# Performance work log

Hardware: AMD Instinct MI355X
Metric: run time of the kernel (lower is better)

The kernel has to match this reference:

```python
import jax, jax.numpy as jnp
import numpy as np

N_STREAM = 5
N_ITER = 5
P_DIMS = [240, 240, 240, 240, 240]
P = sum(P_DIMS)          # 1200
B = 128
KAPPA = 0.8
LEAKY_SLOPE = 0.01       # torch nn.LeakyReLU default


def _build_masks():
    # retrive_it_mask=True: mask[i] = ones over first sum(P_DIMS[:n_stream-i]) dims, zeros after
    rows = []
    for i in range(N_ITER):
        n_on = int(sum(P_DIMS[:N_STREAM - i]))
        rows.append(np.concatenate([np.ones(n_on, np.float32), np.zeros(P - n_on, np.float32)]))
    return jnp.asarray(np.stack(rows))  # [n_iter, P]


def f_p(x):
    # LeakyReLU(clamp(x, -1, 1))
    return jax.nn.leaky_relu(jnp.clip(x, -1.0, 1.0), negative_slope=LEAKY_SLOPE)


def setup_inputs() -> dict:
    key = jax.random.key(0)
    k1, k2 = jax.random.split(key)
    query = jax.random.normal(k1, (B, P), dtype=jnp.float32)
    # scale M so the batched GEMV doesn't saturate the clamp everywhere
    M = jax.random.normal(k2, (B, P, P), dtype=jnp.float32) * (1.0 / np.sqrt(P))
    masks = _build_masks()
    return {"query": query, "M": M, "masks": masks}


def reference(query, M, masks):
    # query: [B, P] (torch.cat of the per-stream list), M: [B, P, P], masks: [n_iter, P]
    h = f_p(query)

    def step(h, mask):
        mv = jnp.einsum('bp,bpq->bq', h, M)            # batched vector-matrix product
        h_new = (1.0 - mask) * h + mask * f_p(KAPPA * h + h * mv)
        return h_new, None

    h, _ = jax.lax.scan(step, h, masks)
    # original returns the per-stream split [h[:, n_p[f]:n_p[f+1]]]; that is a zero-cost
    # view of the concatenated h, so we return the full [B, P] tensor.
    return h
```

## Files before the change

### kernel.cpp

```cpp
#include <hip/hip_runtime.h>

namespace {

constexpr int kB = 128;
constexpr int kP = 1200;
constexpr int kP4 = kP / 4;
constexpr float kKappa = 0.8f;
constexpr float kSlope = 0.01f;

constexpr int kZMax = 16;
constexpr int kBatch = 5;

__device__ __forceinline__ float f_p(float x) {
    x = fminf(1.0f, fmaxf(-1.0f, x));
    return x >= 0.0f ? x : kSlope * x;
}

__global__ __launch_bounds__(256) void init_h(const float* __restrict__ q,
                                              float* __restrict__ h) {
    int i = blockIdx.x * 256 + threadIdx.x;
    if (i < kB * kP) h[i] = f_p(q[i]);
}

__global__ __launch_bounds__(256) void mv_partial(const float* __restrict__ h_in,
                                                  const float* __restrict__ M,
                                                  float* __restrict__ part,
                                                  int n_on, int chunk) {
    const int b = blockIdx.y;
    const int z = blockIdx.z;
    const int tile = blockIdx.x;
    const int tid = threadIdx.x;
    const int wave = tid >> 6;
    const int lane = tid & 63;

    __shared__ float hs[kP / 4 + 4];
    __shared__ float4 red[4][64];

    if ((chunk & 3) == 0) {
        const float4* h4 = (const float4*)(h_in + (size_t)b * kP + z * chunk);
        float4* hs4 = (float4*)hs;
        for (int i = tid; i < chunk / 4; i += 256) hs4[i] = h4[i];
    } else {
        const float* hp = h_in + (size_t)b * kP + z * chunk;
        for (int i = tid; i < chunk; i += 256) hs[i] = hp[i];
    }
    __syncthreads();

    const int cf_max = n_on / 4 - 1;
    const int cf = min(tile * 64 + lane, cf_max);

    const int r0 = (chunk * wave) / 4;
    const int r1 = (chunk * (wave + 1)) / 4;

    const float4* Mp = (const float4*)(M + (size_t)b * kP * kP) +
                       (size_t)(z * chunk + r0) * kP4 + cf;

    float4 acc = make_float4(0.f, 0.f, 0.f, 0.f);
    int r = r0;
    for (; r + kBatch <= r1; r += kBatch) {
        float4 m[kBatch];
        #pragma unroll
        for (int j = 0; j < kBatch; ++j) m[j] = Mp[(size_t)j * kP4];
        float hv[kBatch];
        #pragma unroll
        for (int j = 0; j < kBatch; ++j) hv[j] = hs[r + j];
        #pragma unroll
        for (int j = 0; j < kBatch; ++j) {
            acc.x = fmaf(hv[j], m[j].x, acc.x);
            acc.y = fmaf(hv[j], m[j].y, acc.y);
            acc.z = fmaf(hv[j], m[j].z, acc.z);
            acc.w = fmaf(hv[j], m[j].w, acc.w);
        }
        Mp += (size_t)kBatch * kP4;
    }
    for (; r < r1; ++r) {
        float4 m = *Mp;
        float hv = hs[r];
        acc.x = fmaf(hv, m.x, acc.x);
        acc.y = fmaf(hv, m.y, acc.y);
        acc.z = fmaf(hv, m.z, acc.z);
        acc.w = fmaf(hv, m.w, acc.w);
        Mp += kP4;
    }
    red[wave][lane] = acc;
    __syncthreads();

    const int q = tile * 256 + tid;
    if (q < n_on) {
        const float* pf = (const float*)red;
        float mv = pf[0 * 256 + tid] + pf[1 * 256 + tid] +
                   pf[2 * 256 + tid] + pf[3 * 256 + tid];
        part[((size_t)z * kB + b) * kP + q] = mv;
    }
}

__global__ __launch_bounds__(256) void apply_update(const float* __restrict__ h_in,
                                                    const float* __restrict__ part,
                                                    float* __restrict__ h_out,
                                                    int n_on, int nZ) {
    int i = blockIdx.x * 256 + threadIdx.x;
    if (i >= kB * kP) return;
    const int b = i / kP;
    const int q = i - b * kP;
    float h = h_in[i];
    if (q < n_on) {
        float mv = 0.0f;
        for (int z = 0; z < nZ; ++z)
            mv += part[((size_t)z * kB + b) * kP + q];
        h = f_p(kKappa * h + h * mv);
    }
    h_out[i] = h;
}

__global__ __launch_bounds__(256) void iter_step(const float* __restrict__ h_in,
                                                 const float* __restrict__ M,
                                                 float* __restrict__ h_out,
                                                 int n_on) {
    const int b = blockIdx.y;
    const int tile = blockIdx.x;
    const int tid = threadIdx.x;
    const int wave = tid >> 6;
    const int lane = tid & 63;

    __shared__ float hs[kP];
    __shared__ float4 part[4][64];

    {
        const float4* h4 = (const float4*)(h_in + (size_t)b * kP);
        float4* hs4 = (float4*)hs;
        for (int i = tid; i < kP / 4; i += 256) hs4[i] = h4[i];
    }
    __syncthreads();

    if (tile == 0) {
        for (int i = n_on + tid; i < kP; i += 256)
            h_out[(size_t)b * kP + i] = hs[i];
    }

    const int cf_raw = tile * 64 + lane;
    const int cf = min(cf_raw, kP / 4 - 1);
    const int p0 = wave * 300;

    const float4* Mp = (const float4*)(M + (size_t)b * kP * kP) +
                       (size_t)p0 * (kP / 4) + cf;

    float4 acc = make_float4(0.f, 0.f, 0.f, 0.f);
    for (int pb = 0; pb < 300; pb += 12) {
        float4 m[12];
        #pragma unroll
        for (int j = 0; j < 12; ++j) m[j] = Mp[(size_t)j * (kP / 4)];
        float hv[12];
        #pragma unroll
        for (int j = 0; j < 3; ++j) {
            float4 h4v = *(const float4*)&hs[p0 + pb + j * 4];
            hv[j * 4 + 0] = h4v.x; hv[j * 4 + 1] = h4v.y;
            hv[j * 4 + 2] = h4v.z; hv[j * 4 + 3] = h4v.w;
        }
        #pragma unroll
        for (int j = 0; j < 12; ++j) {
            acc.x = fmaf(hv[j], m[j].x, acc.x);
            acc.y = fmaf(hv[j], m[j].y, acc.y);
            acc.z = fmaf(hv[j], m[j].z, acc.z);
            acc.w = fmaf(hv[j], m[j].w, acc.w);
        }
        Mp += 12 * (kP / 4);
    }
    part[wave][lane] = acc;
    __syncthreads();

    const int q = tile * 256 + tid;
    if (q < n_on) {
        const float* pf = (const float*)part;
        float mv = pf[0 * 256 + tid] + pf[1 * 256 + tid] +
                   pf[2 * 256 + tid] + pf[3 * 256 + tid];
        const float hq = hs[q];
        h_out[(size_t)b * kP + q] = f_p(kKappa * hq + hq * mv);
    }
}

}

extern "C" void kernel_launch(void* const* d_in, const int* in_sizes, int n_in,
                              void* d_out, int out_size, void* d_ws, size_t ws_size,
                              hipStream_t stream) {
    const float* query = (const float*)d_in[0];
    const float* M     = (const float*)d_in[1];
    float* out = (float*)d_out;
    float* w   = (float*)d_ws;

    const int n_on[5] = {1200, 960, 720, 480, 240};
    const size_t kHElems = (size_t)kB * kP;
    const size_t kNeed16 = (size_t)(1 + kZMax) * kHElems * sizeof(float);
    const size_t kNeed4  = (size_t)(1 + 4)     * kHElems * sizeof(float);

    init_h<<<dim3((kB * kP + 255) / 256), dim3(256), 0, stream>>>(query, w);

    if (ws_size >= kNeed4) {
        int zs[5] = {4, 4, 6, 8, 16};
        if (ws_size < kNeed16) { zs[2] = 4; zs[3] = 4; zs[4] = 4; }

        float* hbuf = w;
        float* part = w + kHElems;
        float* bufs[6] = {hbuf, out, hbuf, out, hbuf, out};
        for (int it = 0; it < 5; ++it) {
            const int nZ = zs[it];
            const int chunk = kP / nZ;
            dim3 grid((n_on[it] + 255) / 256, kB, nZ);
            mv_partial<<<grid, dim3(256), 0, stream>>>(bufs[it], M, part,
                                                       n_on[it], chunk);
            apply_update<<<dim3((kB * kP + 255) / 256), dim3(256), 0, stream>>>(
                bufs[it], part, bufs[it + 1], n_on[it], nZ);
        }
    } else {
        float* bufs[6] = {w, out, w, out, w, out};
        for (int it = 0; it < 5; ++it) {
            dim3 grid((n_on[it] + 255) / 256, kB);
            iter_step<<<grid, dim3(256), 0, stream>>>(bufs[it], M, bufs[it + 1], n_on[it]);
        }
    }
}
```

Before: 1.212 ms.

## Restructure batched GEMV so each block walks full rows of a K-chunk

Replaces the column-tiled split-K kernel with a templated kernel where each block owns one batch and one of 8 row-chunks. Threads cover the active column width as float4s and step sequentially through rows, with a row-group count chosen per iteration so narrower iterations still keep threads busy. The aim is to read each M row contiguously across the whole active width, avoid the per-tile h reload and 4-wave shared reduction, and use a fixed Z of 8. In exchange, each iteration's grid is smaller (8×128 blocks) and some threads sit idle in the 320-thread blocks.

```diff
diff --git a/kernel.cpp b/kernel.cpp
--- a/kernel.cpp
+++ b/kernel.cpp
@@ -8,8 +8,9 @@
 constexpr float kKappa = 0.8f;
 constexpr float kSlope = 0.01f;
 
-constexpr int kZMax = 16;
-constexpr int kBatch = 5;
+constexpr int kZ = 8;
+constexpr int kRows = kP / kZ;
+constexpr int kThreads = 320;
 
 __device__ __forceinline__ float f_p(float x) {
     x = fminf(1.0f, fmaxf(-1.0f, x));
@@ -22,75 +23,62 @@
     if (i < kB * kP) h[i] = f_p(q[i]);
 }
 
-__global__ __launch_bounds__(256) void mv_partial(const float* __restrict__ h_in,
-                                                  const float* __restrict__ M,
-                                                  float* __restrict__ part,
-                                                  int n_on, int chunk) {
+template <int N4, int RG>
+__global__ __launch_bounds__(kThreads) void mv_rowseq(const float* __restrict__ h_in,
+                                                      const float* __restrict__ M,
+                                                      float* __restrict__ part) {
+    constexpr int kSteps = (RG == 2) ? 5 : 6;
+    static_assert(kRows % (RG * kSteps) == 0, "batch must divide chunk");
+    constexpr int kActive = N4 * RG;
+    static_assert(kActive <= kThreads, "row-groups must fit the block");
+
+    const int z = blockIdx.x;
     const int b = blockIdx.y;
-    const int z = blockIdx.z;
-    const int tile = blockIdx.x;
     const int tid = threadIdx.x;
-    const int wave = tid >> 6;
-    const int lane = tid & 63;
-
-    __shared__ float hs[kP / 4 + 4];
-    __shared__ float4 red[4][64];
-
-    if ((chunk & 3) == 0) {
-        const float4* h4 = (const float4*)(h_in + (size_t)b * kP + z * chunk);
-        float4* hs4 = (float4*)hs;
-        for (int i = tid; i < chunk / 4; i += 256) hs4[i] = h4[i];
+    const int col = tid % N4;
+    const int rg  = tid / N4;
+
+    __shared__ float hs[kRows];
+
+    if (tid < kRows) hs[tid] = h_in[(size_t)b * kP + z * kRows + tid];
+    __syncthreads();
+
+    float4 acc = make_float4(0.f, 0.f, 0.f, 0.f);
+    if (tid < kActive) {
+        const float4* p = (const float4*)(M + (size_t)b * kP * kP) +
+                          (size_t)(z * kRows + rg) * kP4 + col;
+        for (int r = 0; r < kRows; r += RG * kSteps) {
+            float4 m[kSteps];
+            #pragma unroll
+            for (int j = 0; j < kSteps; ++j) m[j] = p[(size_t)(j * RG) * kP4];
+            #pragma unroll
+            for (int j = 0; j < kSteps; ++j) {
+                const float hv = hs[r + rg + j * RG];
+                acc.x = fmaf(hv, m[j].x, acc.x);
+                acc.y = fmaf(hv, m[j].y, acc.y);
+                acc.z = fmaf(hv, m[j].z, acc.z);
+                acc.w = fmaf(hv, m[j].w, acc.w);
+            }
+            p += (size_t)(RG * kSteps) * kP4;
+        }
+    }
+
+    if constexpr (RG == 1) {
+        if (tid < N4)
+            ((float4*)(part + ((size_t)z * kB + b) * kP))[tid] = acc;
     } else {
-        const float* hp = h_in + (size_t)b * kP + z * chunk;
-        for (int i = tid; i < chunk; i += 256) hs[i] = hp[i];
-    }
-    __syncthreads();
-
-    const int cf_max = n_on / 4 - 1;
-    const int cf = min(tile * 64 + lane, cf_max);
-
-    const int r0 = (chunk * wave) / 4;
-    const int r1 = (chunk * (wave + 1)) / 4;
-
-    const float4* Mp = (const float4*)(M + (size_t)b * kP * kP) +
-                       (size_t)(z * chunk + r0) * kP4 + cf;
-
-    float4 acc = make_float4(0.f, 0.f, 0.f, 0.f);
-    int r = r0;
-    for (; r + kBatch <= r1; r += kBatch) {
-        float4 m[kBatch];
-        #pragma unroll
-        for (int j = 0; j < kBatch; ++j) m[j] = Mp[(size_t)j * kP4];
-        float hv[kBatch];
-        #pragma unroll
-        for (int j = 0; j < kBatch; ++j) hv[j] = hs[r + j];
-        #pragma unroll
-        for (int j = 0; j < kBatch; ++j) {
-            acc.x = fmaf(hv[j], m[j].x, acc.x);
-            acc.y = fmaf(hv[j], m[j].y, acc.y);
-            acc.z = fmaf(hv[j], m[j].z, acc.z);
-            acc.w = fmaf(hv[j], m[j].w, acc.w);
-        }
-        Mp += (size_t)kBatch * kP4;
-    }
-    for (; r < r1; ++r) {
-        float4 m = *Mp;
-        float hv = hs[r];
-        acc.x = fmaf(hv, m.x, acc.x);
-        acc.y = fmaf(hv, m.y, acc.y);
-        acc.z = fmaf(hv, m.z, acc.z);
-        acc.w = fmaf(hv, m.w, acc.w);
-        Mp += kP4;
-    }
-    red[wave][lane] = acc;
-    __syncthreads();
-
-    const int q = tile * 256 + tid;
-    if (q < n_on) {
-        const float* pf = (const float*)red;
-        float mv = pf[0 * 256 + tid] + pf[1 * 256 + tid] +
-                   pf[2 * 256 + tid] + pf[3 * 256 + tid];
-        part[((size_t)z * kB + b) * kP + q] = mv;
+        __shared__ float4 red[kThreads];
+        red[tid] = acc;
+        __syncthreads();
+        if (tid < N4) {
+            float4 s = red[tid];
+            #pragma unroll
+            for (int g = 1; g < RG; ++g) {
+                const float4 t = red[tid + g * N4];
+                s.x += t.x; s.y += t.y; s.z += t.z; s.w += t.w;
+            }
+            ((float4*)(part + ((size_t)z * kB + b) * kP))[tid] = s;
+        }
     }
 }
 
@@ -137,8 +125,7 @@
             h_out[(size_t)b * kP + i] = hs[i];
     }
 
-    const int cf_raw = tile * 64 + lane;
-    const int cf = min(cf_raw, kP / 4 - 1);
+    const int cf = min(tile * 64 + lane, kP / 4 - 1);
     const int p0 = wave * 300;
 
     const float4* Mp = (const float4*)(M + (size_t)b * kP * kP) +
@@ -190,26 +177,26 @@
 
     const int n_on[5] = {1200, 960, 720, 480, 240};
     const size_t kHElems = (size_t)kB * kP;
-    const size_t kNeed16 = (size_t)(1 + kZMax) * kHElems * sizeof(float);
-    const size_t kNeed4  = (size_t)(1 + 4)     * kHElems * sizeof(float);
+    const size_t kNeed = (size_t)(1 + kZ) * kHElems * sizeof(float);
 
     init_h<<<dim3((kB * kP + 255) / 256), dim3(256), 0, stream>>>(query, w);
 
-    if (ws_size >= kNeed4) {
-        int zs[5] = {4, 4, 6, 8, 16};
-        if (ws_size < kNeed16) { zs[2] = 4; zs[3] = 4; zs[4] = 4; }
-
+    if (ws_size >= kNeed) {
         float* hbuf = w;
         float* part = w + kHElems;
         float* bufs[6] = {hbuf, out, hbuf, out, hbuf, out};
+        const dim3 gmv(kZ, kB);
+        const dim3 gap((kB * kP + 255) / 256);
         for (int it = 0; it < 5; ++it) {
-            const int nZ = zs[it];
-            const int chunk = kP / nZ;
-            dim3 grid((n_on[it] + 255) / 256, kB, nZ);
-            mv_partial<<<grid, dim3(256), 0, stream>>>(bufs[it], M, part,
-                                                       n_on[it], chunk);
-            apply_update<<<dim3((kB * kP + 255) / 256), dim3(256), 0, stream>>>(
-                bufs[it], part, bufs[it + 1], n_on[it], nZ);
+            switch (it) {
+                case 0: mv_rowseq<300, 1><<<gmv, kThreads, 0, stream>>>(bufs[it], M, part); break;
+                case 1: mv_rowseq<240, 1><<<gmv, kThreads, 0, stream>>>(bufs[it], M, part); break;
+                case 2: mv_rowseq<180, 1><<<gmv, kThreads, 0, stream>>>(bufs[it], M, part); break;
+                case 3: mv_rowseq<120, 2><<<gmv, kThreads, 0, stream>>>(bufs[it], M, part); break;
+                case 4: mv_rowseq< 60, 5><<<gmv, kThreads, 0, stream>>>(bufs[it], M, part); break;
+            }
+            apply_update<<<gap, dim3(256), 0, stream>>>(bufs[it], part,
+                                                        bufs[it + 1], n_on[it], kZ);
         }
     } else {
         float* bufs[6] = {w, out, w, out, w, out};
```

Measured after the change: 1.214 ms. About the same (+0.2%).
